# Performance work log

Measured on AMD Instinct MI355X. Metric: run time of the kernel, lower is better.

The kernel has to match this reference:

```python
import jax, jax.numpy as jnp
import numpy as np

B, H, S, DH = 2, 16, 2048, 64  # d_model=1024, n_head=16 -> d_head=64


def setup_inputs() -> dict:
    key = jax.random.key(0)
    kq, kk, kv = jax.random.split(key, 3)
    query = jax.random.normal(kq, (B, H, S, DH), dtype=jnp.float32)
    k = jax.random.normal(kk, (B, H, S, DH), dtype=jnp.float32)
    value = jax.random.normal(kv, (B, H, S, DH), dtype=jnp.float32)
    # causal 0/1 float mask, broadcast to the full score shape [B,H,S,S]
    causal = jnp.tril(jnp.ones((S, S), dtype=jnp.float32))
    mask = jnp.broadcast_to(causal, (B, H, S, S))
    return {"query": query, "key": k, "value": value, "mask": mask}


def reference(query, key, value, mask):
    d_head = query.shape[-1]
    # score[b,h,i,j] = q[b,h,i,:] . k[b,h,j,:] / sqrt(d_head)
    score = jnp.einsum('bhid,bhjd->bhij', query, key) / jnp.sqrt(
        jnp.asarray(d_head, dtype=query.dtype))
    score = jnp.where(mask == 0, jnp.asarray(-9e15, dtype=score.dtype), score)
    attn = jax.nn.softmax(score, axis=-1)
    context = jnp.einsum('bhij,bhjd->bhid', attn, value)
    return (context, attn)
```

## Files before the change

### kernel.cpp

```cpp
#include <hip/hip_runtime.h>
#include <hip/hip_bf16.h>

typedef __attribute__((ext_vector_type(8))) __bf16 bf16x8;
typedef __attribute__((ext_vector_type(4))) __bf16 bf16x4;
typedef __attribute__((ext_vector_type(4))) float f32x4;

constexpr int kS  = 2048;
constexpr int kDH = 64;
constexpr int kKT = 64;
constexpr int kLD = 72;
constexpr int kNBH = 32;

__device__ __forceinline__ void tile_barrier() {
    asm volatile("s_waitcnt lgkmcnt(0)" ::: "memory");
    __builtin_amdgcn_s_barrier();
    asm volatile("" ::: "memory");
}

__global__ __launch_bounds__(256)
void prep_k(const float* __restrict__ Kf, __bf16* __restrict__ Kb) {
    const int i = ((int)blockIdx.x * 256 + (int)threadIdx.x) * 8;
    float4 a = *(const float4*)(Kf + i);
    float4 b = *(const float4*)(Kf + i + 4);
    bf16x8 o;
    o[0] = (__bf16)a.x; o[1] = (__bf16)a.y; o[2] = (__bf16)a.z; o[3] = (__bf16)a.w;
    o[4] = (__bf16)b.x; o[5] = (__bf16)b.y; o[6] = (__bf16)b.z; o[7] = (__bf16)b.w;
    *(bf16x8*)(Kb + i) = o;
}

__global__ __launch_bounds__(256)
void prep_v(const float* __restrict__ Vf, __bf16* __restrict__ Vt) {
    __shared__ float Vl[kKT][68];
    const int bh = blockIdx.y, k0 = (int)blockIdx.x * kKT;
    const int tid = (int)threadIdx.x;
    const float* Vb = Vf + (size_t)bh * kS * kDH;
#pragma unroll
    for (int i = 0; i < 4; ++i) {
        const int row = i * 16 + (tid >> 4);
        const int c4  = (tid & 15) * 4;
        *(float4*)&Vl[row][c4] = *(const float4*)(Vb + (size_t)(k0 + row) * kDH + c4);
    }
    __syncthreads();
    const int d = tid >> 2, kg = tid & 3;
    bf16x8 o0, o1;
#pragma unroll
    for (int j = 0; j < 8; ++j) {
        o0[j] = (__bf16)Vl[kg * 16 + j][d];
        o1[j] = (__bf16)Vl[kg * 16 + 8 + j][d];
    }
    __bf16* dst = Vt + (size_t)bh * kDH * kS + (size_t)d * kS + k0 + kg * 16;
    *(bf16x8*)dst = o0;
    *(bf16x8*)(dst + 8) = o1;
}

template<bool WS>
__global__ __launch_bounds__(256)
void sdpa_main(const float* __restrict__ Q, const float* __restrict__ Kf,
               const float* __restrict__ Vf, const __bf16* __restrict__ Kb,
               const __bf16* __restrict__ Vt, float* __restrict__ Cb0,
               float* __restrict__ Ab0)
{
    __shared__ __align__(16) __bf16 Ksh[2][kKT][kLD];
    __shared__ __align__(16) __bf16 Vsh[2][kDH][kLD];
    __shared__ __align__(16) __bf16 Ps[4][16][kLD];

    const int bid   = (int)blockIdx.x;
    const int xcd   = bid & 7;
    const int j     = bid >> 3;
    const int head4 = j >> 5;
    const int i5    = j & 31;
    const int br    = ((i5 & 1) << 4) | ((i5 & 2) << 2) | (i5 & 4)
                    | ((i5 & 8) >> 2) | ((i5 & 16) >> 4);
    const int rb    = (br + head4 * 8) & 31;
    const int bh    = xcd * 4 + head4;
    const int r0    = rb * kKT;

    const int tid  = (int)threadIdx.x;
    const int wave = tid >> 6;
    const int lane = tid & 63;
    const int lr   = lane & 15;
    const int lk   = lane >> 4;
    const int srow = tid >> 4;
    const int sc4  = (tid & 15) * 4;

    const float*  Qb  = Q  + (size_t)bh * kS * kDH;
    const float*  Kfb = Kf + (size_t)bh * kS * kDH;
    const float*  Vfb = Vf + (size_t)bh * kS * kDH;
    const __bf16* Kbb = Kb + (size_t)bh * kS * kDH;
    const __bf16* Vtb = Vt + (size_t)bh * kDH * kS;
    float*        Cb  = Cb0 + (size_t)bh * kS * kDH;
    float*        Ab  = Ab0 + (size_t)bh * kS * kS;

    auto loadK = [&](int t, bf16x4 r[4]) {
#pragma unroll
        for (int i = 0; i < 4; ++i) {
            const int row = i * 16 + srow;
            if constexpr (WS) {
                r[i] = *(const bf16x4*)(Kbb + (size_t)(t * kKT + row) * kDH + sc4);
            } else {
                float4 v = *(const float4*)(Kfb + (size_t)(t * kKT + row) * kDH + sc4);
                r[i][0] = (__bf16)v.x; r[i][1] = (__bf16)v.y;
                r[i][2] = (__bf16)v.z; r[i][3] = (__bf16)v.w;
            }
        }
    };
    auto loadV = [&](int t, bf16x4 r[4]) {
#pragma unroll
        for (int i = 0; i < 4; ++i) {
            const int d = i * 16 + srow;
            if constexpr (WS) {
                r[i] = *(const bf16x4*)(Vtb + (size_t)d * kS + t * kKT + sc4);
            } else {
#pragma unroll
                for (int j2 = 0; j2 < 4; ++j2)
                    r[i][j2] = (__bf16)Vfb[(size_t)(t * kKT + sc4 + j2) * kDH + d];
            }
        }
    };
    auto storeK = [&](int buf, const bf16x4 r[4]) {
#pragma unroll
        for (int i = 0; i < 4; ++i)
            *(bf16x4*)&Ksh[buf][i * 16 + srow][sc4] = r[i];
    };
    auto storeV = [&](int buf, const bf16x4 r[4]) {
#pragma unroll
        for (int i = 0; i < 4; ++i)
            *(bf16x4*)&Vsh[buf][i * 16 + srow][sc4] = r[i];
    };

    {
        const int cstart = (rb + 1) * kKT;
        const int n4 = (kS - cstart) >> 2;
        if (n4 > 0) {
            const f32x4 z = {0.f, 0.f, 0.f, 0.f};
            for (int r = 0; r < kKT; ++r) {
                f32x4* p = (f32x4*)(Ab + (size_t)(r0 + r) * kS + cstart);
                for (int i = tid; i < n4; i += 256)
                    __builtin_nontemporal_store(z, p + i);
            }
        }
    }

    const int qrow = r0 + wave * 16 + lr;
    bf16x8 qf[2];
#pragma unroll
    for (int ch = 0; ch < 2; ++ch) {
        const float* qp = Qb + (size_t)qrow * kDH + ch * 32 + lk * 8;
        float4 a = *(const float4*)qp;
        float4 b = *(const float4*)(qp + 4);
        qf[ch][0] = (__bf16)(a.x * 0.125f);
        qf[ch][1] = (__bf16)(a.y * 0.125f);
        qf[ch][2] = (__bf16)(a.z * 0.125f);
        qf[ch][3] = (__bf16)(a.w * 0.125f);
        qf[ch][4] = (__bf16)(b.x * 0.125f);
        qf[ch][5] = (__bf16)(b.y * 0.125f);
        qf[ch][6] = (__bf16)(b.z * 0.125f);
        qf[ch][7] = (__bf16)(b.w * 0.125f);
    }

    float lsum = 0.f;
    {
        bf16x4 kreg[4];
        loadK(0, kreg);
        storeK(0, kreg);
        __syncthreads();
        for (int t = 0; t <= rb; ++t) {
            const int cur = t & 1;
            if (t < rb) loadK(t + 1, kreg);
            const int c0 = t * kKT;
#pragma unroll
            for (int cf = 0; cf < 4; ++cf) {
                bf16x8 a0 = *(const bf16x8*)&Ksh[cur][cf * 16 + lr][lk * 8];
                bf16x8 a1 = *(const bf16x8*)&Ksh[cur][cf * 16 + lr][32 + lk * 8];
                f32x4 acc = {0.f, 0.f, 0.f, 0.f};
                __builtin_amdgcn_s_setprio(1);
                acc = __builtin_amdgcn_mfma_f32_16x16x32_bf16(a0, qf[0], acc, 0, 0, 0);
                acc = __builtin_amdgcn_mfma_f32_16x16x32_bf16(a1, qf[1], acc, 0, 0, 0);
                __builtin_amdgcn_s_setprio(0);
#pragma unroll
                for (int r = 0; r < 4; ++r) {
                    const int key = c0 + cf * 16 + lk * 4 + r;
                    lsum += __expf((key > qrow) ? -1e30f : acc[r]);
                }
            }
            if (t < rb) {
                storeK(cur ^ 1, kreg);
                tile_barrier();
            }
        }
    }
    lsum += __shfl_xor(lsum, 16);
    lsum += __shfl_xor(lsum, 32);
    const float il = 1.f / lsum;

    f32x4 ctx[4] = {{0.f,0.f,0.f,0.f},{0.f,0.f,0.f,0.f},{0.f,0.f,0.f,0.f},{0.f,0.f,0.f,0.f}};

    __syncthreads();
    {
        bf16x4 kreg[4], vreg[4];
        loadK(0, kreg);
        loadV(0, vreg);
        storeK(0, kreg);
        storeV(0, vreg);
        __syncthreads();
        for (int t = 0; t <= rb; ++t) {
            const int cur = t & 1;
            if (t < rb) { loadK(t + 1, kreg); loadV(t + 1, vreg); }
            const int c0 = t * kKT;
#pragma unroll
            for (int cf = 0; cf < 4; ++cf) {
                bf16x8 a0 = *(const bf16x8*)&Ksh[cur][cf * 16 + lr][lk * 8];
                bf16x8 a1 = *(const bf16x8*)&Ksh[cur][cf * 16 + lr][32 + lk * 8];
                f32x4 acc = {0.f, 0.f, 0.f, 0.f};
                __builtin_amdgcn_s_setprio(1);
                acc = __builtin_amdgcn_mfma_f32_16x16x32_bf16(a0, qf[0], acc, 0, 0, 0);
                acc = __builtin_amdgcn_mfma_f32_16x16x32_bf16(a1, qf[1], acc, 0, 0, 0);
                __builtin_amdgcn_s_setprio(0);
                bf16x4 pb;
#pragma unroll
                for (int r = 0; r < 4; ++r) {
                    const int key = c0 + cf * 16 + lk * 4 + r;
                    float p = __expf(acc[r]) * il;
                    if (key > qrow) p = 0.f;
                    pb[r] = (__bf16)p;
                }
                *(bf16x4*)&Ps[wave][lr][cf * 16 + lk * 4] = pb;
            }

            bf16x8 pa0 = *(const bf16x8*)&Ps[wave][lr][lk * 8];
            bf16x8 pa1 = *(const bf16x8*)&Ps[wave][lr][32 + lk * 8];
            __builtin_amdgcn_s_setprio(1);
#pragma unroll
            for (int df = 0; df < 4; ++df) {
                bf16x8 w0 = *(const bf16x8*)&Vsh[cur][df * 16 + lr][lk * 8];
                bf16x8 w1 = *(const bf16x8*)&Vsh[cur][df * 16 + lr][32 + lk * 8];
                ctx[df] = __builtin_amdgcn_mfma_f32_16x16x32_bf16(pa0, w0, ctx[df], 0, 0, 0);
                ctx[df] = __builtin_amdgcn_mfma_f32_16x16x32_bf16(pa1, w1, ctx[df], 0, 0, 0);
            }
            __builtin_amdgcn_s_setprio(0);

#pragma unroll
            for (int it = 0; it < 4; ++it) {
                const int row = it * 4 + (lane >> 4);
                const int c4  = (lane & 15) * 4;
                bf16x4 pv4 = *(const bf16x4*)&Ps[wave][row][c4];
                f32x4 o = {(float)pv4[0], (float)pv4[1], (float)pv4[2], (float)pv4[3]};
                *(f32x4*)(Ab + (size_t)(r0 + wave * 16 + row) * kS + c0 + c4) = o;
            }

            if (t < rb) {
                storeK(cur ^ 1, kreg);
                storeV(cur ^ 1, vreg);
                tile_barrier();
            }
        }
    }

#pragma unroll
    for (int df = 0; df < 4; ++df) {
#pragma unroll
        for (int r = 0; r < 4; ++r) {
            const int rowg = r0 + wave * 16 + lk * 4 + r;
            Cb[(size_t)rowg * kDH + df * 16 + lr] = ctx[df][r];
        }
    }
}

extern "C" void kernel_launch(void* const* d_in, const int* in_sizes, int n_in,
                              void* d_out, int out_size, void* d_ws, size_t ws_size,
                              hipStream_t stream) {
    (void)in_sizes; (void)n_in; (void)out_size;
    const float* Q = (const float*)d_in[0];
    const float* K = (const float*)d_in[1];
    const float* V = (const float*)d_in[2];
    float* ctx  = (float*)d_out;
    float* attn = ctx + (size_t)kNBH * kS * kDH;

    const size_t elems = (size_t)kNBH * kS * kDH;
    const size_t need  = 2 * elems * sizeof(__bf16);
    if (ws_size >= need) {
        __bf16* Kb = (__bf16*)d_ws;
        __bf16* Vt = Kb + elems;
        prep_k<<<dim3((unsigned)(elems / (8 * 256))), dim3(256), 0, stream>>>(K, Kb);
        prep_v<<<dim3(kS / kKT, kNBH), dim3(256), 0, stream>>>(V, Vt);
        sdpa_main<true><<<dim3(1024), dim3(256), 0, stream>>>(Q, K, V, Kb, Vt, ctx, attn);
    } else {
        sdpa_main<false><<<dim3(1024), dim3(256), 0, stream>>>(Q, K, V, nullptr, nullptr, ctx, attn);
    }
}
```

Measured before the change: 173.3 us.

## Interleave zero-fill of masked attention region into the softmax-sum pass

The upfront loop that zeroed the causally masked part of the attention matrix is removed. Those zero stores are now spread across the iterations of the first key pass, so the write traffic overlaps with MFMA and exp work instead of running serially before it. The change also splits the row-sum accumulator into four independent partial sums to shorten the dependency chain, makes the attention and context stores nontemporal, and swaps __syncthreads for the lighter tile barrier. The work split (mq per iteration) must cover every masked column, otherwise some entries are left unwritten.

Measured after the change: 197.5 us. +14.0%, slower.

```diff
diff --git a/kernel.cpp b/kernel.cpp
--- a/kernel.cpp
+++ b/kernel.cpp
@@ -128,18 +128,12 @@
             *(bf16x4*)&Vsh[buf][i * 16 + srow][sc4] = r[i];
     };
 
-    {
-        const int cstart = (rb + 1) * kKT;
-        const int n4 = (kS - cstart) >> 2;
-        if (n4 > 0) {
-            const f32x4 z = {0.f, 0.f, 0.f, 0.f};
-            for (int r = 0; r < kKT; ++r) {
-                f32x4* p = (f32x4*)(Ab + (size_t)(r0 + r) * kS + cstart);
-                for (int i = tid; i < n4; i += 256)
-                    __builtin_nontemporal_store(z, p + i);
-            }
-        }
-    }
+    const int cstart = (rb + 1) * kKT;
+    const int n4row  = (kS - cstart) >> 2;
+    const int M      = n4row >> 2;
+    const int mq     = (M + rb) / (rb + 1);
+    float* fillp = Ab + (size_t)(r0 + (tid >> 2)) * kS + cstart + (tid & 3) * 4;
+    const f32x4 z4 = {0.f, 0.f, 0.f, 0.f};
 
     const int qrow = r0 + wave * 16 + lr;
     bf16x8 qf[2];
@@ -158,15 +152,20 @@
         qf[ch][7] = (__bf16)(b.w * 0.125f);
     }
 
-    float lsum = 0.f;
+    float ls4[4] = {0.f, 0.f, 0.f, 0.f};
     {
         bf16x4 kreg[4];
         loadK(0, kreg);
         storeK(0, kreg);
-        __syncthreads();
+        tile_barrier();
         for (int t = 0; t <= rb; ++t) {
             const int cur = t & 1;
             if (t < rb) loadK(t + 1, kreg);
+            {
+                const int m1 = min((t + 1) * mq, M);
+                for (int m = t * mq; m < m1; ++m)
+                    __builtin_nontemporal_store(z4, (f32x4*)(fillp + 16 * m));
+            }
             const int c0 = t * kKT;
 #pragma unroll
             for (int cf = 0; cf < 4; ++cf) {
@@ -180,7 +179,7 @@
 #pragma unroll
                 for (int r = 0; r < 4; ++r) {
                     const int key = c0 + cf * 16 + lk * 4 + r;
-                    lsum += __expf((key > qrow) ? -1e30f : acc[r]);
+                    ls4[r] += __expf((key > qrow) ? -1e30f : acc[r]);
                 }
             }
             if (t < rb) {
@@ -189,20 +188,21 @@
             }
         }
     }
+    float lsum = (ls4[0] + ls4[1]) + (ls4[2] + ls4[3]);
     lsum += __shfl_xor(lsum, 16);
     lsum += __shfl_xor(lsum, 32);
     const float il = 1.f / lsum;
 
     f32x4 ctx[4] = {{0.f,0.f,0.f,0.f},{0.f,0.f,0.f,0.f},{0.f,0.f,0.f,0.f},{0.f,0.f,0.f,0.f}};
 
-    __syncthreads();
+    tile_barrier();
     {
         bf16x4 kreg[4], vreg[4];
         loadK(0, kreg);
         loadV(0, vreg);
         storeK(0, kreg);
         storeV(0, vreg);
-        __syncthreads();
+        tile_barrier();
         for (int t = 0; t <= rb; ++t) {
             const int cur = t & 1;
             if (t < rb) { loadK(t + 1, kreg); loadV(t + 1, vreg); }
@@ -245,7 +245,8 @@
                 const int c4  = (lane & 15) * 4;
                 bf16x4 pv4 = *(const bf16x4*)&Ps[wave][row][c4];
                 f32x4 o = {(float)pv4[0], (float)pv4[1], (float)pv4[2], (float)pv4[3]};
-                *(f32x4*)(Ab + (size_t)(r0 + wave * 16 + row) * kS + c0 + c4) = o;
+                __builtin_nontemporal_store(o,
+                    (f32x4*)(Ab + (size_t)(r0 + wave * 16 + row) * kS + c0 + c4));
             }
 
             if (t < rb) {
@@ -261,7 +262,7 @@
 #pragma unroll
         for (int r = 0; r < 4; ++r) {
             const int rowg = r0 + wave * 16 + lk * 4 + r;
-            Cb[(size_t)rowg * kDH + df * 16 + lr] = ctx[df][r];
+            __builtin_nontemporal_store(ctx[df][r], Cb + (size_t)rowg * kDH + df * 16 + lr);
         }
     }
 }
```

## Interleave masked-zero fill with first pass and store fp32 probabilities directly

Applied to the files above, without the earlier changes.

The upper-triangle zero fill of the attention matrix is no longer a separate loop before compute. It is now spread across the iterations of the first (row-sum) pass so the stores overlap with the MFMA and exp work. The attention output is written straight from registers as fp32 before bf16 rounding, which removes the LDS read-back and conversion loop, though the per-lane store pattern is less coalesced (16-byte chunks scattered across rows). The row-sum is also split into four independent accumulators to shorten the dependency chain.

Result: no change. 171.2 us (-1.2%).

```diff
diff --git a/kernel.cpp b/kernel.cpp
--- a/kernel.cpp
+++ b/kernel.cpp
@@ -128,18 +128,10 @@
             *(bf16x4*)&Vsh[buf][i * 16 + srow][sc4] = r[i];
     };
 
-    {
-        const int cstart = (rb + 1) * kKT;
-        const int n4 = (kS - cstart) >> 2;
-        if (n4 > 0) {
-            const f32x4 z = {0.f, 0.f, 0.f, 0.f};
-            for (int r = 0; r < kKT; ++r) {
-                f32x4* p = (f32x4*)(Ab + (size_t)(r0 + r) * kS + cstart);
-                for (int i = tid; i < n4; i += 256)
-                    __builtin_nontemporal_store(z, p + i);
-            }
-        }
-    }
+    const int cstart = (rb + 1) * kKT;
+    const int n4row  = (kS - cstart) >> 2;
+    const int rt     = (kKT + rb) / (rb + 1);
+    const f32x4 z4 = {0.f, 0.f, 0.f, 0.f};
 
     const int qrow = r0 + wave * 16 + lr;
     bf16x8 qf[2];
@@ -158,7 +150,7 @@
         qf[ch][7] = (__bf16)(b.w * 0.125f);
     }
 
-    float lsum = 0.f;
+    float ls4[4] = {0.f, 0.f, 0.f, 0.f};
     {
         bf16x4 kreg[4];
         loadK(0, kreg);
@@ -167,6 +159,15 @@
         for (int t = 0; t <= rb; ++t) {
             const int cur = t & 1;
             if (t < rb) loadK(t + 1, kreg);
+            if (n4row > 0) {
+                const int rA = t * rt;
+                const int rB = min(rA + rt, kKT);
+                for (int r = rA; r < rB; ++r) {
+                    f32x4* p = (f32x4*)(Ab + (size_t)(r0 + r) * kS + cstart);
+                    for (int i = tid; i < n4row; i += 256)
+                        __builtin_nontemporal_store(z4, p + i);
+                }
+            }
             const int c0 = t * kKT;
 #pragma unroll
             for (int cf = 0; cf < 4; ++cf) {
@@ -180,7 +181,7 @@
 #pragma unroll
                 for (int r = 0; r < 4; ++r) {
                     const int key = c0 + cf * 16 + lk * 4 + r;
-                    lsum += __expf((key > qrow) ? -1e30f : acc[r]);
+                    ls4[r] += __expf((key > qrow) ? -1e30f : acc[r]);
                 }
             }
             if (t < rb) {
@@ -189,6 +190,7 @@
             }
         }
     }
+    float lsum = (ls4[0] + ls4[1]) + (ls4[2] + ls4[3]);
     lsum += __shfl_xor(lsum, 16);
     lsum += __shfl_xor(lsum, 32);
     const float il = 1.f / lsum;
@@ -216,14 +218,17 @@
                 acc = __builtin_amdgcn_mfma_f32_16x16x32_bf16(a0, qf[0], acc, 0, 0, 0);
                 acc = __builtin_amdgcn_mfma_f32_16x16x32_bf16(a1, qf[1], acc, 0, 0, 0);
                 __builtin_amdgcn_s_setprio(0);
+                f32x4 pn;
                 bf16x4 pb;
 #pragma unroll
                 for (int r = 0; r < 4; ++r) {
                     const int key = c0 + cf * 16 + lk * 4 + r;
                     float p = __expf(acc[r]) * il;
                     if (key > qrow) p = 0.f;
+                    pn[r] = p;
                     pb[r] = (__bf16)p;
                 }
+                *(f32x4*)(Ab + (size_t)qrow * kS + c0 + cf * 16 + lk * 4) = pn;
                 *(bf16x4*)&Ps[wave][lr][cf * 16 + lk * 4] = pb;
             }
 
@@ -238,15 +243,6 @@
                 ctx[df] = __builtin_amdgcn_mfma_f32_16x16x32_bf16(pa1, w1, ctx[df], 0, 0, 0);
             }
             __builtin_amdgcn_s_setprio(0);
-
-#pragma unroll
-            for (int it = 0; it < 4; ++it) {
-                const int row = it * 4 + (lane >> 4);
-                const int c4  = (lane & 15) * 4;
-                bf16x4 pv4 = *(const bf16x4*)&Ps[wave][row][c4];
-                f32x4 o = {(float)pv4[0], (float)pv4[1], (float)pv4[2], (float)pv4[3]};
-                *(f32x4*)(Ab + (size_t)(r0 + wave * 16 + row) * kS + c0 + c4) = o;
-            }
 
             if (t < rb) {
                 storeK(cur ^ 1, kreg);
```

## Stage K/V tiles via global_load_lds with XOR-swizzled LDS layout

Applied to the files above, without the earlier changes.

Replaces the register-staged K/V tile copies with direct global-to-LDS loads (global_load_lds) in the workspace path. The bf16 K and transposed V are pre-swizzled in the prep kernels so that the padded LDS rows can be dropped in favour of an XOR-swizzled layout that avoids bank conflicts. The attention-probability store now writes fp32 values straight from registers instead of re-reading the bf16 Ps tile, which also changes the stored attn values from bf16-rounded to full fp32. The custom lgkmcnt barrier is replaced by __syncthreads, which must also cover completion of the async LDS loads, a correctness risk if the vmcnt wait is not implied.

After: 167.9 us, median of 2. 3.1% less time.

```diff
diff --git a/kernel.cpp b/kernel.cpp
--- a/kernel.cpp
+++ b/kernel.cpp
@@ -8,24 +8,28 @@
 constexpr int kS  = 2048;
 constexpr int kDH = 64;
 constexpr int kKT = 64;
-constexpr int kLD = 72;
 constexpr int kNBH = 32;
 
-__device__ __forceinline__ void tile_barrier() {
-    asm volatile("s_waitcnt lgkmcnt(0)" ::: "memory");
-    __builtin_amdgcn_s_barrier();
-    asm volatile("" ::: "memory");
+__device__ __forceinline__ void gload16(const __bf16* g, __bf16* l) {
+    __builtin_amdgcn_global_load_lds(
+        (const __attribute__((address_space(1))) void*)g,
+        (__attribute__((address_space(3))) void*)l,
+        16, 0, 0);
 }
 
 __global__ __launch_bounds__(256)
 void prep_k(const float* __restrict__ Kf, __bf16* __restrict__ Kb) {
-    const int i = ((int)blockIdx.x * 256 + (int)threadIdx.x) * 8;
-    float4 a = *(const float4*)(Kf + i);
-    float4 b = *(const float4*)(Kf + i + 4);
+    const int gid = (int)blockIdx.x * 256 + (int)threadIdx.x;
+    const int key = gid >> 3;
+    const int g   = gid & 7;
+    const int gs  = g ^ (key & 7);
+    const float* src = Kf + (size_t)key * kDH + gs * 8;
+    float4 a = *(const float4*)src;
+    float4 b = *(const float4*)(src + 4);
     bf16x8 o;
     o[0] = (__bf16)a.x; o[1] = (__bf16)a.y; o[2] = (__bf16)a.z; o[3] = (__bf16)a.w;
     o[4] = (__bf16)b.x; o[5] = (__bf16)b.y; o[6] = (__bf16)b.z; o[7] = (__bf16)b.w;
-    *(bf16x8*)(Kb + i) = o;
+    *(bf16x8*)(Kb + (size_t)key * kDH + g * 8) = o;
 }
 
 __global__ __launch_bounds__(256)
@@ -48,9 +52,11 @@
         o0[j] = (__bf16)Vl[kg * 16 + j][d];
         o1[j] = (__bf16)Vl[kg * 16 + 8 + j][d];
     }
-    __bf16* dst = Vt + (size_t)bh * kDH * kS + (size_t)d * kS + k0 + kg * 16;
-    *(bf16x8*)dst = o0;
-    *(bf16x8*)(dst + 8) = o1;
+    const int i0 = (2 * kg)     ^ (d & 7);
+    const int i1 = (2 * kg + 1) ^ (d & 7);
+    __bf16* dst = Vt + (size_t)bh * kDH * kS + (size_t)d * kS + k0;
+    *(bf16x8*)(dst + i0 * 8) = o0;
+    *(bf16x8*)(dst + i1 * 8) = o1;
 }
 
 template<bool WS>
@@ -60,9 +66,9 @@
                const __bf16* __restrict__ Vt, float* __restrict__ Cb0,
                float* __restrict__ Ab0)
 {
-    __shared__ __align__(16) __bf16 Ksh[2][kKT][kLD];
-    __shared__ __align__(16) __bf16 Vsh[2][kDH][kLD];
-    __shared__ __align__(16) __bf16 Ps[4][16][kLD];
+    __shared__ __align__(16) __bf16 KshL[2][kKT * 64];
+    __shared__ __align__(16) __bf16 VshL[2][kDH * 64];
+    __shared__ __align__(16) __bf16 PsL[4][16 * 64];
 
     const int bid   = (int)blockIdx.x;
     const int xcd   = bid & 7;
@@ -80,6 +86,7 @@
     const int lane = tid & 63;
     const int lr   = lane & 15;
     const int lk   = lane >> 4;
+    const int sw   = lr & 7;
     const int srow = tid >> 4;
     const int sc4  = (tid & 15) * 4;
 
@@ -91,41 +98,50 @@
     float*        Cb  = Cb0 + (size_t)bh * kS * kDH;
     float*        Ab  = Ab0 + (size_t)bh * kS * kS;
 
+    auto stageK = [&](int t, int buf) {
+        const __bf16* s0 = Kbb + (size_t)(t * kKT + wave * 16 + (lane >> 3)) * kDH + (lane & 7) * 8;
+        __bf16* d0 = &KshL[buf][(wave * 16) * 64];
+        gload16(s0, d0);
+        gload16(s0 + 8 * kDH, d0 + 8 * 64);
+    };
+    auto stageV = [&](int t, int buf) {
+        const __bf16* s0 = Vtb + (size_t)(wave * 16 + (lane >> 3)) * kS + t * kKT + (lane & 7) * 8;
+        __bf16* d0 = &VshL[buf][(wave * 16) * 64];
+        gload16(s0, d0);
+        gload16(s0 + 8 * kS, d0 + 8 * 64);
+    };
+
     auto loadK = [&](int t, bf16x4 r[4]) {
+#pragma unroll
+        for (int i = 0; i < 4; ++i) {
+            float4 v = *(const float4*)(Kfb + (size_t)(t * kKT + i * 16 + srow) * kDH + sc4);
+            r[i][0] = (__bf16)v.x; r[i][1] = (__bf16)v.y;
+            r[i][2] = (__bf16)v.z; r[i][3] = (__bf16)v.w;
+        }
+    };
+    auto loadV = [&](int t, bf16x4 r[4]) {
+#pragma unroll
+        for (int i = 0; i < 4; ++i) {
+            const int d = i * 16 + srow;
+#pragma unroll
+            for (int j2 = 0; j2 < 4; ++j2)
+                r[i][j2] = (__bf16)Vfb[(size_t)(t * kKT + sc4 + j2) * kDH + d];
+        }
+    };
+    const int sg = (tid & 15) >> 1, sh = tid & 1;
+    auto storeKL = [&](int buf, const bf16x4 r[4]) {
 #pragma unroll
         for (int i = 0; i < 4; ++i) {
             const int row = i * 16 + srow;
-            if constexpr (WS) {
-                r[i] = *(const bf16x4*)(Kbb + (size_t)(t * kKT + row) * kDH + sc4);
-            } else {
-                float4 v = *(const float4*)(Kfb + (size_t)(t * kKT + row) * kDH + sc4);
-                r[i][0] = (__bf16)v.x; r[i][1] = (__bf16)v.y;
-                r[i][2] = (__bf16)v.z; r[i][3] = (__bf16)v.w;
-            }
-        }
-    };
-    auto loadV = [&](int t, bf16x4 r[4]) {
+            *(bf16x4*)&KshL[buf][row * 64 + ((sg ^ (row & 7)) << 3) + (sh << 2)] = r[i];
+        }
+    };
+    auto storeVL = [&](int buf, const bf16x4 r[4]) {
 #pragma unroll
         for (int i = 0; i < 4; ++i) {
             const int d = i * 16 + srow;
-            if constexpr (WS) {
-                r[i] = *(const bf16x4*)(Vtb + (size_t)d * kS + t * kKT + sc4);
-            } else {
-#pragma unroll
-                for (int j2 = 0; j2 < 4; ++j2)
-                    r[i][j2] = (__bf16)Vfb[(size_t)(t * kKT + sc4 + j2) * kDH + d];
-            }
-        }
-    };
-    auto storeK = [&](int buf, const bf16x4 r[4]) {
-#pragma unroll
-        for (int i = 0; i < 4; ++i)
-            *(bf16x4*)&Ksh[buf][i * 16 + srow][sc4] = r[i];
-    };
-    auto storeV = [&](int buf, const bf16x4 r[4]) {
-#pragma unroll
-        for (int i = 0; i < 4; ++i)
-            *(bf16x4*)&Vsh[buf][i * 16 + srow][sc4] = r[i];
+            *(bf16x4*)&VshL[buf][d * 64 + ((sg ^ (d & 7)) << 3) + (sh << 2)] = r[i];
+        }
     };
 
     {
@@ -160,18 +176,27 @@
 
     float lsum = 0.f;
     {
-        bf16x4 kreg[4];
-        loadK(0, kreg);
-        storeK(0, kreg);
+        if constexpr (WS) {
+            stageK(0, 0);
+        } else {
+            bf16x4 kreg0[4];
+            loadK(0, kreg0);
+            storeKL(0, kreg0);
+        }
         __syncthreads();
         for (int t = 0; t <= rb; ++t) {
             const int cur = t & 1;
-            if (t < rb) loadK(t + 1, kreg);
+            bf16x4 kreg[4];
+            if (t < rb) {
+                if constexpr (WS) stageK(t + 1, cur ^ 1);
+                else loadK(t + 1, kreg);
+            }
             const int c0 = t * kKT;
 #pragma unroll
             for (int cf = 0; cf < 4; ++cf) {
-                bf16x8 a0 = *(const bf16x8*)&Ksh[cur][cf * 16 + lr][lk * 8];
-                bf16x8 a1 = *(const bf16x8*)&Ksh[cur][cf * 16 + lr][32 + lk * 8];
+                const __bf16* kb = &KshL[cur][(cf * 16 + lr) * 64];
+                bf16x8 a0 = *(const bf16x8*)(kb + ((lk ^ sw) << 3));
+                bf16x8 a1 = *(const bf16x8*)(kb + (((lk + 4) ^ sw) << 3));
                 f32x4 acc = {0.f, 0.f, 0.f, 0.f};
                 __builtin_amdgcn_s_setprio(1);
                 acc = __builtin_amdgcn_mfma_f32_16x16x32_bf16(a0, qf[0], acc, 0, 0, 0);
@@ -184,8 +209,8 @@
                 }
             }
             if (t < rb) {
-                storeK(cur ^ 1, kreg);
-                tile_barrier();
+                if constexpr (!WS) storeKL(cur ^ 1, kreg);
+                __syncthreads();
             }
         }
     }
@@ -197,61 +222,73 @@
 
     __syncthreads();
     {
-        bf16x4 kreg[4], vreg[4];
-        loadK(0, kreg);
-        loadV(0, vreg);
-        storeK(0, kreg);
-        storeV(0, vreg);
+        if constexpr (WS) {
+            stageK(0, 0);
+            stageV(0, 0);
+        } else {
+            bf16x4 kreg0[4], vreg0[4];
+            loadK(0, kreg0);
+            loadV(0, vreg0);
+            storeKL(0, kreg0);
+            storeVL(0, vreg0);
+        }
         __syncthreads();
         for (int t = 0; t <= rb; ++t) {
             const int cur = t & 1;
-            if (t < rb) { loadK(t + 1, kreg); loadV(t + 1, vreg); }
+            bf16x4 kreg[4], vreg[4];
+            if (t < rb) {
+                if constexpr (WS) {
+                    stageK(t + 1, cur ^ 1);
+                    stageV(t + 1, cur ^ 1);
+                } else {
+                    loadK(t + 1, kreg);
+                    loadV(t + 1, vreg);
+                }
+            }
             const int c0 = t * kKT;
 #pragma unroll
             for (int cf = 0; cf < 4; ++cf) {
-                bf16x8 a0 = *(const bf16x8*)&Ksh[cur][cf * 16 + lr][lk * 8];
-                bf16x8 a1 = *(const bf16x8*)&Ksh[cur][cf * 16 + lr][32 + lk * 8];
+                const __bf16* kb = &KshL[cur][(cf * 16 + lr) * 64];
+                bf16x8 a0 = *(const bf16x8*)(kb + ((lk ^ sw) << 3));
+                bf16x8 a1 = *(const bf16x8*)(kb + (((lk + 4) ^ sw) << 3));
                 f32x4 acc = {0.f, 0.f, 0.f, 0.f};
                 __builtin_amdgcn_s_setprio(1);
                 acc = __builtin_amdgcn_mfma_f32_16x16x32_bf16(a0, qf[0], acc, 0, 0, 0);
                 acc = __builtin_amdgcn_mfma_f32_16x16x32_bf16(a1, qf[1], acc, 0, 0, 0);
                 __builtin_amdgcn_s_setprio(0);
+                f32x4 pn;
                 bf16x4 pb;
 #pragma unroll
                 for (int r = 0; r < 4; ++r) {
                     const int key = c0 + cf * 16 + lk * 4 + r;
                     float p = __expf(acc[r]) * il;
                     if (key > qrow) p = 0.f;
+                    pn[r] = p;
                     pb[r] = (__bf16)p;
                 }
-                *(bf16x4*)&Ps[wave][lr][cf * 16 + lk * 4] = pb;
-            }
-
-            bf16x8 pa0 = *(const bf16x8*)&Ps[wave][lr][lk * 8];
-            bf16x8 pa1 = *(const bf16x8*)&Ps[wave][lr][32 + lk * 8];
+                *(f32x4*)(Ab + (size_t)qrow * kS + c0 + cf * 16 + lk * 4) = pn;
+                *(bf16x4*)&PsL[wave][lr * 64 + (((2 * cf + (lk >> 1)) ^ sw) << 3) + ((lk & 1) << 2)] = pb;
+            }
+
+            bf16x8 pa0 = *(const bf16x8*)&PsL[wave][lr * 64 + ((lk ^ sw) << 3)];
+            bf16x8 pa1 = *(const bf16x8*)&PsL[wave][lr * 64 + (((lk + 4) ^ sw) << 3)];
             __builtin_amdgcn_s_setprio(1);
 #pragma unroll
             for (int df = 0; df < 4; ++df) {
-                bf16x8 w0 = *(const bf16x8*)&Vsh[cur][df * 16 + lr][lk * 8];
-                bf16x8 w1 = *(const bf16x8*)&Vsh[cur][df * 16 + lr][32 + lk * 8];
+                const __bf16* vb = &VshL[cur][(df * 16 + lr) * 64];
+                bf16x8 w0 = *(const bf16x8*)(vb + ((lk ^ sw) << 3));
+                bf16x8 w1 = *(const bf16x8*)(vb + (((lk + 4) ^ sw) << 3));
                 ctx[df] = __builtin_amdgcn_mfma_f32_16x16x32_bf16(pa0, w0, ctx[df], 0, 0, 0);
                 ctx[df] = __builtin_amdgcn_mfma_f32_16x16x32_bf16(pa1, w1, ctx[df], 0, 0, 0);
             }
             __builtin_amdgcn_s_setprio(0);
 
-#pragma unroll
-            for (int it = 0; it < 4; ++it) {
-                const int row = it * 4 + (lane >> 4);
-                const int c4  = (lane & 15) * 4;
-                bf16x4 pv4 = *(const bf16x4*)&Ps[wave][row][c4];
-                f32x4 o = {(float)pv4[0], (float)pv4[1], (float)pv4[2], (float)pv4[3]};
-                *(f32x4*)(Ab + (size_t)(r0 + wave * 16 + row) * kS + c0 + c4) = o;
-            }
-
             if (t < rb) {
-                storeK(cur ^ 1, kreg);
-                storeV(cur ^ 1, vreg);
-                tile_barrier();
+                if constexpr (!WS) {
+                    storeKL(cur ^ 1, kreg);
+                    storeVL(cur ^ 1, vreg);
+                }
+                __syncthreads();
             }
         }
     }
```
